# Performance work log

Measured on AMD Instinct MI355X. Metric: run time of the kernel, lower is better.

## Reference

```python
import jax, jax.numpy as jnp
import numpy as np


def setup_inputs() -> dict:
    key = jax.random.key(0)
    k1, k2 = jax.random.split(key)
    B, M, N = 16, 4096, 4096
    target_points = jax.random.normal(k1, (B, M, 2), dtype=jnp.float32)
    actual_points = jax.random.normal(k2, (B, N, 2), dtype=jnp.float32)
    return {"target_points": target_points, "actual_points": actual_points}


def reference(target_points, actual_points):
    # target_points: [B, M, 2], actual_points: [B, N, 2]
    # diff[b, m, n] = || target[b, m] - actual[b, n] ||_2
    d = target_points[:, :, None, :] - actual_points[:, None, :, :]  # [B, M, N, 2]
    diff = jnp.sqrt(jnp.sum(d * d, axis=-1))  # [B, M, N]
    forward_loss = jnp.min(diff, axis=2)   # [B, M] nearest actual for each target
    backward_loss = jnp.min(diff, axis=1)  # [B, N] nearest target for each actual
    return (forward_loss, backward_loss)
```

## Files before the change

### kernel.cpp

```cpp
#include <hip/hip_runtime.h>
#include <math.h>


#define BLK 256
#define TM  8
#define RC  32
#define UNR 4

__global__ __launch_bounds__(256) void chamfer_init(unsigned int* __restrict__ out, int n) {
    int i = blockIdx.x * 256 + threadIdx.x;
    if (i < n) out[i] = 0x7F800000u;
}

__global__ __launch_bounds__(BLK) void chamfer_partial(
    const float2* __restrict__ tpts,
    const float2* __restrict__ apts,
    unsigned int* __restrict__ out,
    int M, int N, int B)
{
    const int b   = blockIdx.y;
    const int zc  = blockIdx.z;
    const int dir = zc & 1;
    const int rc  = zc >> 1;

    const float2* __restrict__ Q = dir ? apts : tpts;
    const float2* __restrict__ R = dir ? tpts : apts;
    const int NQ = dir ? N : M;
    const int NR = dir ? M : N;
    unsigned int* __restrict__ o =
        out + (dir ? ((size_t)B * M + (size_t)b * N) : ((size_t)b * M));

    const float2* __restrict__ q = Q + (size_t)b * NQ;
    const float2* __restrict__ r = R + (size_t)b * NR;

    const int clen = (NR + RC - 1) / RC;
    const int rbeg = rc * clen;
    const int rend = (rbeg + clen < NR) ? (rbeg + clen) : NR;
    if (rbeg >= rend) return;

    int   qi[TM];
    float n2x[TM], n2y[TM], qn[TM], mn[TM];
#pragma unroll
    for (int k = 0; k < TM; ++k) {
        qi[k] = blockIdx.x * (BLK * TM) + k * BLK + (int)threadIdx.x;
        int idx = qi[k] < NQ ? qi[k] : NQ - 1;
        float2 p = q[idx];
        n2x[k] = -2.0f * p.x;
        n2y[k] = -2.0f * p.y;
        qn[k]  = fmaf(p.y, p.y, p.x * p.x);
        mn[k]  = 3.0e38f;
    }

    int n = rbeg;
    for (; n + UNR <= rend; n += UNR) {
        float vx[UNR], vy[UNR], va[UNR];
#pragma unroll
        for (int j = 0; j < UNR; ++j) {
            float2 p = r[n + j];
            vx[j] = p.x; vy[j] = p.y;
            va[j] = fmaf(p.y, p.y, p.x * p.x);
        }
#pragma unroll
        for (int k = 0; k < TM; ++k) {
            float v0 = fmaf(n2x[k], vx[0], fmaf(n2y[k], vy[0], va[0]));
            float v1 = fmaf(n2x[k], vx[1], fmaf(n2y[k], vy[1], va[1]));
            float v2 = fmaf(n2x[k], vx[2], fmaf(n2y[k], vy[2], va[2]));
            float v3 = fmaf(n2x[k], vx[3], fmaf(n2y[k], vy[3], va[3]));
            float t  = fminf(fminf(v0, v1), v2);
            mn[k]    = fminf(fminf(t, v3), mn[k]);
        }
    }
    for (; n < rend; ++n) {
        float2 p = r[n];
        float va = fmaf(p.y, p.y, p.x * p.x);
#pragma unroll
        for (int k = 0; k < TM; ++k) {
            float v = fmaf(n2x[k], p.x, fmaf(n2y[k], p.y, va));
            mn[k] = fminf(mn[k], v);
        }
    }

#pragma unroll
    for (int k = 0; k < TM; ++k) {
        if (qi[k] < NQ) {
            float d2 = fmaxf(mn[k] + qn[k], 0.0f);
            atomicMin(&o[qi[k]], __float_as_uint(d2));
        }
    }
}

__global__ __launch_bounds__(256) void chamfer_sqrt(
    unsigned int* __restrict__ io, int n)
{
    int i = blockIdx.x * 256 + threadIdx.x;
    if (i < n) {
        float d2 = __uint_as_float(io[i]);
        ((float*)io)[i] = sqrtf(d2);
    }
}

extern "C" void kernel_launch(void* const* d_in, const int* in_sizes, int n_in,
                              void* d_out, int out_size, void* d_ws, size_t ws_size,
                              hipStream_t stream) {
    const float2* tpts = (const float2*)d_in[0];
    const float2* apts = (const float2*)d_in[1];
    unsigned int* out = (unsigned int*)d_out;

    const int B = 16;
    const int M = in_sizes[0] / (B * 2);
    const int N = in_sizes[1] / (B * 2);
    const int total = B * (M + N);

    chamfer_init<<<(total + 255) / 256, 256, 0, stream>>>(out, total);

    const int maxQ = M > N ? M : N;
    dim3 grid((maxQ + BLK * TM - 1) / (BLK * TM), B, 2 * RC);
    chamfer_partial<<<grid, dim3(BLK), 0, stream>>>(tpts, apts, out, M, N, B);

    chamfer_sqrt<<<(total + 255) / 256, 256, 0, stream>>>(out, total);
}
```

Before: 49.01 us.

## Replace brute-force chamfer with uniform-grid nearest-neighbor search

Adds a spatial-hash path: each point set is binned into a 64x64 uniform grid over [-5,5] with per-cell buckets and an overflow list. Each query then searches expanding rings of cells until the best distance is within the ring bound, and finally scans the overflow list. This replaces the quadratic all-pairs scan with near-constant work per query, at the cost of atomics during build, divergent loops, and a large workspace. The old brute-force path is kept as a fallback, with an 8-wide unrolled inner loop, float4 loads and v_min3 reductions.

```diff
diff --git a/kernel.cpp b/kernel.cpp
--- a/kernel.cpp
+++ b/kernel.cpp
@@ -1,11 +1,135 @@
 #include <hip/hip_runtime.h>
 #include <math.h>
 
+
+#define G     64
+#define GG    (G * G)
+#define CAP   64
+#define OCAP  4096
+#define CELLW 0.15625f
+#define INVW  6.4f
+#define NSETS 32
+
+__global__ __launch_bounds__(256) void grid_zero(unsigned int* __restrict__ cnts, int n) {
+    int i = blockIdx.x * 256 + threadIdx.x;
+    if (i < n) cnts[i] = 0u;
+}
+
+__global__ __launch_bounds__(256) void grid_build(
+    const float2* __restrict__ tpts, const float2* __restrict__ apts,
+    unsigned int* __restrict__ counts,
+    unsigned int* __restrict__ ovfcnt,
+    float2* __restrict__ buckets,
+    float2* __restrict__ ovf,
+    int M, int N, int B)
+{
+    int idx = blockIdx.x * 256 + threadIdx.x;
+    int total = B * (M + N);
+    if (idx >= total) return;
+
+    int s; float2 p;
+    if (idx < B * M) { s = idx / M;             p = tpts[idx]; }
+    else             { int j = idx - B * M; s = B + j / N; p = apts[j]; }
+
+    int cx = (int)floorf((p.x + 5.0f) * INVW);
+    int cy = (int)floorf((p.y + 5.0f) * INVW);
+    cx = cx < 0 ? 0 : (cx > G - 1 ? G - 1 : cx);
+    cy = cy < 0 ? 0 : (cy > G - 1 ? G - 1 : cy);
+    int c = s * GG + cy * G + cx;
+
+    unsigned slot = atomicAdd(&counts[c], 1u);
+    if (slot < CAP) {
+        buckets[(size_t)c * CAP + slot] = p;
+    } else {
+        unsigned o = atomicAdd(&ovfcnt[s], 1u);
+        if (o < OCAP) ovf[(size_t)s * OCAP + o] = p;
+    }
+}
+
+__global__ __launch_bounds__(256) void grid_query(
+    const float2* __restrict__ tpts, const float2* __restrict__ apts,
+    const unsigned int* __restrict__ counts,
+    const unsigned int* __restrict__ ovfcnt,
+    const float2* __restrict__ buckets,
+    const float2* __restrict__ ovf,
+    float* __restrict__ out, int M, int N, int B)
+{
+    int tq = blockIdx.x * 256 + threadIdx.x;
+    int total = B * (M + N);
+    if (tq >= total) return;
+
+    int rs; float2 q; size_t oidx;
+    if (tq < B * M) {
+        int b = tq / M;
+        q = tpts[tq];
+        rs = B + b;
+        oidx = (size_t)tq;
+    } else {
+        int j = tq - B * M;
+        int b = j / N;
+        q = apts[j];
+        rs = b;
+        oidx = (size_t)B * M + j;
+    }
+
+    float qx = q.x, qy = q.y;
+    int cx = (int)floorf((qx + 5.0f) * INVW);
+    int cy = (int)floorf((qy + 5.0f) * INVW);
+    cx = cx < 0 ? 0 : (cx > G - 1 ? G - 1 : cx);
+    cy = cy < 0 ? 0 : (cy > G - 1 ? G - 1 : cy);
+
+    const unsigned int* __restrict__ scnt = counts + (size_t)rs * GG;
+    const float2* __restrict__ sbkt = buckets + (size_t)rs * GG * CAP;
+
+    float best = 3.0e38f;
+
+    for (int r = 0; r <= G; ++r) {
+        for (int dy = -r; dy <= r; ++dy) {
+            int yy = cy + dy;
+            if ((unsigned)yy >= (unsigned)G) continue;
+            int rowb = yy * G;
+            int x0, x1, step;
+            if (dy == -r || dy == r) { x0 = cx - r; x1 = cx + r; step = 1; }
+            else                     { x0 = cx - r; x1 = cx + r; step = 2 * r; }
+            if (x0 < 0) x0 = (step == 1) ? 0 : x1;
+            for (int xx = x0; xx <= x1; xx += step) {
+                if ((unsigned)xx >= (unsigned)G) continue;
+                int c = rowb + xx;
+                unsigned cnt = scnt[c];
+                if (cnt > CAP) cnt = CAP;
+                const float2* __restrict__ bp = sbkt + (size_t)c * CAP;
+                for (unsigned j = 0; j < cnt; ++j) {
+                    float2 p = bp[j];
+                    float dx = qx - p.x, dyf = qy - p.y;
+                    best = fminf(best, fmaf(dx, dx, dyf * dyf));
+                }
+            }
+        }
+        float bound = (float)r * CELLW;
+        if (best <= bound * bound) break;
+    }
+
+    unsigned oc = ovfcnt[rs];
+    if (oc > OCAP) oc = OCAP;
+    const float2* __restrict__ op = ovf + (size_t)rs * OCAP;
+    for (unsigned j = 0; j < oc; ++j) {
+        float2 p = op[j];
+        float dx = qx - p.x, dyf = qy - p.y;
+        best = fminf(best, fmaf(dx, dx, dyf * dyf));
+    }
+
+    out[oidx] = sqrtf(best);
+}
 
 #define BLK 256
 #define TM  8
 #define RC  32
-#define UNR 4
+
+__device__ __forceinline__ float min3f(float a, float b, float c) {
+    float d;
+    asm("v_min3_f32 %0, %1, %2, %3" : "=v"(d) : "v"(a), "v"(b), "v"(c));
+    return d;
+}
 
 __global__ __launch_bounds__(256) void chamfer_init(unsigned int* __restrict__ out, int n) {
     int i = blockIdx.x * 256 + threadIdx.x;
@@ -13,90 +137,69 @@
 }
 
 __global__ __launch_bounds__(BLK) void chamfer_partial(
-    const float2* __restrict__ tpts,
-    const float2* __restrict__ apts,
-    unsigned int* __restrict__ out,
-    int M, int N, int B)
+    const float2* __restrict__ tpts, const float2* __restrict__ apts,
+    unsigned int* __restrict__ out, int M, int N, int B)
 {
-    const int b   = blockIdx.y;
-    const int zc  = blockIdx.z;
-    const int dir = zc & 1;
-    const int rc  = zc >> 1;
-
+    const int b = blockIdx.y, zc = blockIdx.z;
+    const int dir = zc & 1, rc = zc >> 1;
     const float2* __restrict__ Q = dir ? apts : tpts;
     const float2* __restrict__ R = dir ? tpts : apts;
-    const int NQ = dir ? N : M;
-    const int NR = dir ? M : N;
+    const int NQ = dir ? N : M, NR = dir ? M : N;
     unsigned int* __restrict__ o =
         out + (dir ? ((size_t)B * M + (size_t)b * N) : ((size_t)b * M));
-
     const float2* __restrict__ q = Q + (size_t)b * NQ;
     const float2* __restrict__ r = R + (size_t)b * NR;
-
     const int clen = (NR + RC - 1) / RC;
     const int rbeg = rc * clen;
     const int rend = (rbeg + clen < NR) ? (rbeg + clen) : NR;
     if (rbeg >= rend) return;
-
-    int   qi[TM];
-    float n2x[TM], n2y[TM], qn[TM], mn[TM];
+    int qi[TM]; float n2x[TM], n2y[TM], qn[TM], mn[TM];
 #pragma unroll
     for (int k = 0; k < TM; ++k) {
         qi[k] = blockIdx.x * (BLK * TM) + k * BLK + (int)threadIdx.x;
         int idx = qi[k] < NQ ? qi[k] : NQ - 1;
         float2 p = q[idx];
-        n2x[k] = -2.0f * p.x;
-        n2y[k] = -2.0f * p.y;
-        qn[k]  = fmaf(p.y, p.y, p.x * p.x);
-        mn[k]  = 3.0e38f;
-    }
-
+        n2x[k] = -2.0f * p.x; n2y[k] = -2.0f * p.y;
+        qn[k] = fmaf(p.y, p.y, p.x * p.x); mn[k] = 3.0e38f;
+    }
     int n = rbeg;
-    for (; n + UNR <= rend; n += UNR) {
-        float vx[UNR], vy[UNR], va[UNR];
-#pragma unroll
-        for (int j = 0; j < UNR; ++j) {
-            float2 p = r[n + j];
-            vx[j] = p.x; vy[j] = p.y;
-            va[j] = fmaf(p.y, p.y, p.x * p.x);
+    for (; n + 8 <= rend; n += 8) {
+        float vx[8], vy[8], va[8];
+#pragma unroll
+        for (int g = 0; g < 4; ++g) {
+            float4 p4 = *(const float4*)&r[n + 2 * g];
+            vx[2*g] = p4.x; vy[2*g] = p4.y; vx[2*g+1] = p4.z; vy[2*g+1] = p4.w;
+            va[2*g]   = fmaf(p4.y, p4.y, p4.x * p4.x);
+            va[2*g+1] = fmaf(p4.w, p4.w, p4.z * p4.z);
         }
 #pragma unroll
         for (int k = 0; k < TM; ++k) {
-            float v0 = fmaf(n2x[k], vx[0], fmaf(n2y[k], vy[0], va[0]));
-            float v1 = fmaf(n2x[k], vx[1], fmaf(n2y[k], vy[1], va[1]));
-            float v2 = fmaf(n2x[k], vx[2], fmaf(n2y[k], vy[2], va[2]));
-            float v3 = fmaf(n2x[k], vx[3], fmaf(n2y[k], vy[3], va[3]));
-            float t  = fminf(fminf(v0, v1), v2);
-            mn[k]    = fminf(fminf(t, v3), mn[k]);
+            float v[8];
+#pragma unroll
+            for (int j = 0; j < 8; ++j)
+                v[j] = fmaf(n2x[k], vx[j], fmaf(n2y[k], vy[j], va[j]));
+            float m = min3f(v[0], v[1], v[2]);
+            m = min3f(m, v[3], v[4]);
+            m = min3f(m, v[5], v[6]);
+            mn[k] = min3f(m, v[7], mn[k]);
         }
     }
     for (; n < rend; ++n) {
         float2 p = r[n];
         float va = fmaf(p.y, p.y, p.x * p.x);
 #pragma unroll
-        for (int k = 0; k < TM; ++k) {
-            float v = fmaf(n2x[k], p.x, fmaf(n2y[k], p.y, va));
-            mn[k] = fminf(mn[k], v);
-        }
-    }
-
-#pragma unroll
-    for (int k = 0; k < TM; ++k) {
-        if (qi[k] < NQ) {
-            float d2 = fmaxf(mn[k] + qn[k], 0.0f);
-            atomicMin(&o[qi[k]], __float_as_uint(d2));
-        }
-    }
-}
-
-__global__ __launch_bounds__(256) void chamfer_sqrt(
-    unsigned int* __restrict__ io, int n)
-{
+        for (int k = 0; k < TM; ++k)
+            mn[k] = fminf(mn[k], fmaf(n2x[k], p.x, fmaf(n2y[k], p.y, va)));
+    }
+#pragma unroll
+    for (int k = 0; k < TM; ++k)
+        if (qi[k] < NQ)
+            atomicMin(&o[qi[k]], __float_as_uint(fmaxf(mn[k] + qn[k], 0.0f)));
+}
+
+__global__ __launch_bounds__(256) void chamfer_sqrt(unsigned int* __restrict__ io, int n) {
     int i = blockIdx.x * 256 + threadIdx.x;
-    if (i < n) {
-        float d2 = __uint_as_float(io[i]);
-        ((float*)io)[i] = sqrtf(d2);
-    }
+    if (i < n) ((float*)io)[i] = sqrtf(__uint_as_float(io[i]));
 }
 
 extern "C" void kernel_launch(void* const* d_in, const int* in_sizes, int n_in,
@@ -104,18 +207,35 @@
                               hipStream_t stream) {
     const float2* tpts = (const float2*)d_in[0];
     const float2* apts = (const float2*)d_in[1];
-    unsigned int* out = (unsigned int*)d_out;
 
     const int B = 16;
     const int M = in_sizes[0] / (B * 2);
     const int N = in_sizes[1] / (B * 2);
     const int total = B * (M + N);
 
-    chamfer_init<<<(total + 255) / 256, 256, 0, stream>>>(out, total);
-
-    const int maxQ = M > N ? M : N;
-    dim3 grid((maxQ + BLK * TM - 1) / (BLK * TM), B, 2 * RC);
-    chamfer_partial<<<grid, dim3(BLK), 0, stream>>>(tpts, apts, out, M, N, B);
-
-    chamfer_sqrt<<<(total + 255) / 256, 256, 0, stream>>>(out, total);
-}
+    size_t cnt_elems = (size_t)NSETS * GG + NSETS;
+    size_t cnt_bytes = cnt_elems * sizeof(unsigned int);
+    size_t bkt_bytes = (size_t)NSETS * GG * CAP * sizeof(float2);
+    size_t ovf_bytes = (size_t)NSETS * OCAP * sizeof(float2);
+    size_t need = cnt_bytes + bkt_bytes + ovf_bytes;
+
+    if (ws_size >= need && M <= OCAP && N <= OCAP) {
+        unsigned int* counts = (unsigned int*)d_ws;
+        unsigned int* ovfcnt = counts + (size_t)NSETS * GG;
+        float2* buckets = (float2*)((char*)d_ws + cnt_bytes);
+        float2* ovf = buckets + (size_t)NSETS * GG * CAP;
+
+        grid_zero<<<((int)cnt_elems + 255) / 256, 256, 0, stream>>>(counts, (int)cnt_elems);
+        grid_build<<<(total + 255) / 256, 256, 0, stream>>>(
+            tpts, apts, counts, ovfcnt, buckets, ovf, M, N, B);
+        grid_query<<<(total + 255) / 256, 256, 0, stream>>>(
+            tpts, apts, counts, ovfcnt, buckets, ovf, (float*)d_out, M, N, B);
+    } else {
+        unsigned int* out = (unsigned int*)d_out;
+        chamfer_init<<<(total + 255) / 256, 256, 0, stream>>>(out, total);
+        const int S = M > N ? M : N;
+        dim3 grid((S + BLK * TM - 1) / (BLK * TM), B, 2 * RC);
+        chamfer_partial<<<grid, dim3(BLK), 0, stream>>>(tpts, apts, out, M, N, B);
+        chamfer_sqrt<<<(total + 255) / 256, 256, 0, stream>>>(out, total);
+    }
+}
```

Measured after the change: 143.7 us. 2.93x slower.
